# Optimization experiments

Hardware: AMD Instinct MI355X
Metric: run time of the kernel (lower is better)

Reference implementation:

```python
import math
import jax, jax.numpy as jnp
import numpy as np

B, H, S, D = 2, 16, 2048, 64


def setup_inputs() -> dict:
    key = jax.random.key(0)
    kq, kk, kv = jax.random.split(key, 3)
    Q = jax.random.normal(kq, (B, H, S, D), dtype=jnp.float32)
    K = jax.random.normal(kk, (B, H, S, D), dtype=jnp.float32)
    V = jax.random.normal(kv, (B, H, S, D), dtype=jnp.float32)
    # padding mask: (N, H, query_len), True = keep (module expands with [..., None])
    padding_mask = jnp.ones((B, H, S), dtype=bool)
    # boolean causal attention mask, broadcastable to (B, H, S, S)
    attention_mask = jnp.tril(jnp.ones((S, S), dtype=bool))[None, None]
    return {"Q": Q, "K": K, "V": V,
            "padding_mask": padding_mask, "attention_mask": attention_mask}


def reference(Q, K, V, padding_mask, attention_mask):
    # scores: (B, H, S_q, S_k)
    scale = 1.0 / math.sqrt(K.shape[-1])
    attn = jnp.einsum("bhqd,bhkd->bhqk", Q, K) * scale
    # query-side padding mask (is_query_mask=True): expand last axis
    attn = jnp.where(padding_mask[..., None], attn, -jnp.inf)
    # boolean attention mask
    attn = jnp.where(attention_mask, attn, -jnp.inf)
    attn = jax.nn.softmax(attn, axis=-1)
    # nan-clean: rows fully masked to -inf softmax to NaN -> 0
    attn = jnp.where(jnp.isnan(attn), 0.0, attn)
    return jnp.einsum("bhqk,bhkd->bhqd", attn, V)
```

## Files before the change

kernel.cpp:

```cpp
#include <hip/hip_runtime.h>


typedef __attribute__((ext_vector_type(8))) short bf16x8;
typedef __attribute__((ext_vector_type(4))) float f32x4;
typedef __attribute__((ext_vector_type(2))) unsigned uint2v;
typedef __attribute__((ext_vector_type(4))) unsigned uint4v;

#define MFMA16(a, b, c) __builtin_amdgcn_mfma_f32_16x16x32_bf16(a, b, c, 0, 0, 0)

#define S_LEN 2048
#define D_DIM 64
#define NBH 32

static __device__ __forceinline__ short f2bf(float f) {
  unsigned u = __builtin_bit_cast(unsigned, f);
  u += 0x7fffu + ((u >> 16) & 1u);
  return (short)(u >> 16);
}

static __device__ __forceinline__ unsigned pk2(float a, float b) {
#if __has_builtin(__builtin_amdgcn_cvt_pk_bf16_f32)
  auto r = __builtin_amdgcn_cvt_pk_bf16_f32(a, b);
  return __builtin_bit_cast(unsigned, r);
#else
  return (unsigned)(unsigned short)f2bf(a) |
         ((unsigned)(unsigned short)f2bf(b) << 16);
#endif
}

static __device__ __forceinline__ float fexp2(float x) {
#if __has_builtin(__builtin_amdgcn_exp2f)
  return __builtin_amdgcn_exp2f(x);
#else
  return exp2f(x);
#endif
}

static __device__ __forceinline__ bf16x8 cvt8(const float* p) {
  f32x4 a = *(const f32x4*)p;
  f32x4 b = *(const f32x4*)(p + 4);
  bf16x8 r;
#pragma unroll
  for (int j = 0; j < 4; ++j) { r[j] = f2bf(a[j]); r[j + 4] = f2bf(b[j]); }
  return r;
}

static __device__ __forceinline__ void load_lds16(const short* g, short* l) {
  __builtin_amdgcn_global_load_lds(
      (const __attribute__((address_space(1))) unsigned*)g,
      (__attribute__((address_space(3))) unsigned*)l, 16, 0, 0);
}

__global__ __launch_bounds__(256) void stage(const float* __restrict__ K,
                                             const float* __restrict__ V,
                                             short* __restrict__ Kb,
                                             short* __restrict__ Vt) {
  const int tid = threadIdx.x;
  if (blockIdx.x < 1024) {
    const size_t b0 = (size_t)blockIdx.x * 4096;
#pragma unroll
    for (int p = 0; p < 2; ++p) {
      const size_t i = b0 + p * 2048 + tid * 8;
      f32x4 a = *(const f32x4*)(K + i);
      f32x4 b = *(const f32x4*)(K + i + 4);
      bf16x8 r;
#pragma unroll
      for (int j = 0; j < 4; ++j) { r[j] = f2bf(a[j]); r[j + 4] = f2bf(b[j]); }
      *(bf16x8*)(Kb + i) = r;
    }
  } else {
    __shared__ unsigned t[64][18];
    const int bi = blockIdx.x - 1024;
    const int bh = bi >> 6, k32 = bi & 63;
    const float* src = V + ((size_t)bh * S_LEN + k32 * 32) * D_DIM;
    const int pr = tid & 15;
    const int dq = tid >> 4;
    f32x4 a = *(const f32x4*)(src + (2 * pr)     * D_DIM + dq * 4);
    f32x4 b = *(const f32x4*)(src + (2 * pr + 1) * D_DIM + dq * 4);
#pragma unroll
    for (int j = 0; j < 4; ++j) t[dq * 4 + j][pr] = pk2(a[j], b[j]);
    __syncthreads();
    const int d = tid >> 2, g = tid & 3;
    uint2v lo = *(const uint2v*)(&t[d][2 * g]);
    uint2v hi = *(const uint2v*)(&t[d][8 + 2 * g]);
    short* dst = Vt + (size_t)bh * D_DIM * S_LEN + (size_t)d * S_LEN +
                 k32 * 32 + g * 8;
    *(uint2v*)(dst)     = lo;
    *(uint2v*)(dst + 4) = hi;
  }
}

__global__ __launch_bounds__(512, 2) void attn_fwd(
    const float* __restrict__ Q, const short* __restrict__ Kb,
    const short* __restrict__ Vt, float* __restrict__ O) {
  __shared__ __align__(16) short kbuf[3][4096];
  __shared__ __align__(16) short vbuf[3][4096];

  const int tid  = threadIdx.x;
  const int wave = tid >> 6;
  const int cid  = wave >> 2;
  const int wq   = wave & 3;
  const int lane = tid & 63;
  const int quad = lane >> 4;
  const int col  = lane & 15;

  const int bh = blockIdx.x & 31;
  const int i2 = blockIdx.x >> 5;
  const int s = i2 & 7, g = i2 >> 3;
  const int p = g ? (15 - s) : s;
  const int qb   = 2 * p + cid;
  const int nblk = 2 * p + 2;
  const int q0 = qb * 64 + wq * 16;

  const float* Qh = Q  + (size_t)bh * S_LEN * D_DIM;
  const short* Kh = Kb + (size_t)bh * S_LEN * D_DIM;
  const short* Vh = Vt + (size_t)bh * D_DIM * S_LEN;

  const bf16x8 bq0 = cvt8(Qh + (size_t)(q0 + col) * D_DIM + quad * 8);
  const bf16x8 bq1 = cvt8(Qh + (size_t)(q0 + col) * D_DIM + quad * 8 + 32);

  const int r0s = tid >> 3, c0s = (tid & 7) ^ (r0s & 7);
  const int wb = wave * 512;

  f32x4 o[4];
#pragma unroll
  for (int i = 0; i < 4; ++i) o[i] = 0.f;
  float psum = 0.f;
  const float sc = 0.125f * 1.44269504088896340736f;

  const int rbase = col * 64;
  const int sw0 = ((quad       ^ (col & 7)) << 3);
  const int sw1 = (((4 + quad) ^ (col & 7)) << 3);

  auto prefetch = [&](int t, int buf) {
    const int k0n = t << 6;
    load_lds16(Kh + (size_t)(k0n + r0s) * 64 + c0s * 8, &kbuf[buf][wb]);
    load_lds16(Vh + (size_t)r0s * S_LEN + k0n + c0s * 8, &vbuf[buf][wb]);
  };

  auto body = [&](int t, bool masked, int buf) {
    const short* kb = kbuf[buf];
    const short* vb = vbuf[buf];

    bf16x8 ak0[4], ak1[4], av0[4], av1[4];
#pragma unroll
    for (int mt = 0; mt < 4; ++mt) {
      ak0[mt] = *(const bf16x8*)(kb + mt * 1024 + rbase + sw0);
      ak1[mt] = *(const bf16x8*)(kb + mt * 1024 + rbase + sw1);
    }
#pragma unroll
    for (int mt = 0; mt < 4; ++mt) {
      av0[mt] = *(const bf16x8*)(vb + mt * 1024 + rbase + sw0);
      av1[mt] = *(const bf16x8*)(vb + mt * 1024 + rbase + sw1);
    }

    f32x4 s4[4];
#pragma unroll
    for (int mt = 0; mt < 4; ++mt) {
      f32x4 c = 0.f;
      c = MFMA16(ak0[mt], bq0, c);
      c = MFMA16(ak1[mt], bq1, c);
      s4[mt] = c;
    }

    unsigned u[8];
    const int k0 = t << 6, qA = q0 + col;
#pragma unroll
    for (int mt = 0; mt < 4; ++mt) {
      float p0 = fexp2(fmaf(s4[mt][0], sc, -8.0f));
      float p1 = fexp2(fmaf(s4[mt][1], sc, -8.0f));
      float p2 = fexp2(fmaf(s4[mt][2], sc, -8.0f));
      float p3 = fexp2(fmaf(s4[mt][3], sc, -8.0f));
      if (masked) {
        const int kk = k0 + mt * 16 + quad * 4;
        if (kk     > qA) p0 = 0.f;
        if (kk + 1 > qA) p1 = 0.f;
        if (kk + 2 > qA) p2 = 0.f;
        if (kk + 3 > qA) p3 = 0.f;
      }
      psum += (p0 + p1) + (p2 + p3);
      u[2 * mt]     = pk2(p0, p1);
      u[2 * mt + 1] = pk2(p2, p3);
    }

    uint4v dv0, dv1;
    dv0[0] = u[0]; dv0[1] = u[1]; dv0[2] = u[2]; dv0[3] = u[3];
    dv1[0] = u[4]; dv1[1] = u[5]; dv1[2] = u[6]; dv1[3] = u[7];
    const bf16x8 bp0 = __builtin_bit_cast(bf16x8, dv0);
    const bf16x8 bp1 = __builtin_bit_cast(bf16x8, dv1);

#pragma unroll
    for (int mt = 0; mt < 4; ++mt) o[mt] = MFMA16(av0[mt], bp0, o[mt]);
#pragma unroll
    for (int mt = 0; mt < 4; ++mt) o[mt] = MFMA16(av1[mt], bp1, o[mt]);
  };

  prefetch(0, 0);
  prefetch(1, 1);
  int cur = 0;
  for (int t = 0; t < nblk; ++t) {
    if (t + 1 < nblk) {
      asm volatile("s_waitcnt vmcnt(2)" ::: "memory");
    } else {
      asm volatile("s_waitcnt vmcnt(0)" ::: "memory");
    }
    __builtin_amdgcn_s_barrier();
    if (t + 2 < nblk) {
      int nb = cur + 2; if (nb >= 3) nb -= 3;
      prefetch(t + 2, nb);
    }
    if (t <= qb) body(t, t == qb, cur);
    if (++cur == 3) cur = 0;
  }

  psum += __shfl_xor(psum, 16);
  psum += __shfl_xor(psum, 32);
  const float rl = 1.f / psum;
  float* op = O + (size_t)bh * S_LEN * D_DIM + (size_t)(q0 + col) * D_DIM;
#pragma unroll
  for (int mt = 0; mt < 4; ++mt) {
    f32x4 ov;
#pragma unroll
    for (int r = 0; r < 4; ++r) ov[r] = o[mt][r] * rl;
    *(f32x4*)(op + mt * 16 + quad * 4) = ov;
  }
}

extern "C" void kernel_launch(void* const* d_in, const int* in_sizes, int n_in,
                              void* d_out, int out_size, void* d_ws, size_t ws_size,
                              hipStream_t stream) {
  const float* Q = (const float*)d_in[0];
  const float* K = (const float*)d_in[1];
  const float* V = (const float*)d_in[2];
  short* Kb = (short*)d_ws;
  short* Vt = Kb + (size_t)NBH * S_LEN * D_DIM;
  stage   <<<dim3(3072), dim3(256), 0, stream>>>(K, V, Kb, Vt);
  attn_fwd<<<dim3(512),  dim3(512), 0, stream>>>(Q, Kb, Vt, (float*)d_out);
}
```

Before: 145.5 us.

## Software-pipeline QK^T one tile ahead with 4-deep LDS ring buffer

Splits the per-tile body into a QK^T stage and a softmax/PV stage, so the QK^T MFMAs for tile t+1 are issued before the exp and PV work of tile t, using ping-pong score registers. The LDS ring grows from 3 to 4 buffers and the prefetch distance from 2 to 3 tiles. The aim is to overlap MFMA work with the exp/convert work and to hide more global-to-LDS latency. In exchange it uses more LDS per block (64KB), which could limit the 2-blocks-per-CU occupancy, and it keeps more live registers.

Result: no change. 145.2 us (-0.2%).

```diff
diff --git a/kernel.cpp b/kernel.cpp
--- a/kernel.cpp
+++ b/kernel.cpp
@@ -93,8 +93,8 @@
 __global__ __launch_bounds__(512, 2) void attn_fwd(
     const float* __restrict__ Q, const short* __restrict__ Kb,
     const short* __restrict__ Vt, float* __restrict__ O) {
-  __shared__ __align__(16) short kbuf[3][4096];
-  __shared__ __align__(16) short vbuf[3][4096];
+  __shared__ __align__(16) short kbuf[4][4096];
+  __shared__ __align__(16) short vbuf[4][4096];
 
   const int tid  = threadIdx.x;
   const int wave = tid >> 6;
@@ -132,37 +132,35 @@
   const int sw0 = ((quad       ^ (col & 7)) << 3);
   const int sw1 = (((4 + quad) ^ (col & 7)) << 3);
 
-  auto prefetch = [&](int t, int buf) {
+  auto prefetch = [&](int t) {
     const int k0n = t << 6;
-    load_lds16(Kh + (size_t)(k0n + r0s) * 64 + c0s * 8, &kbuf[buf][wb]);
-    load_lds16(Vh + (size_t)r0s * S_LEN + k0n + c0s * 8, &vbuf[buf][wb]);
-  };
-
-  auto body = [&](int t, bool masked, int buf) {
-    const short* kb = kbuf[buf];
-    const short* vb = vbuf[buf];
-
-    bf16x8 ak0[4], ak1[4], av0[4], av1[4];
+    short* kd = &kbuf[t & 3][wb];
+    short* vd = &vbuf[t & 3][wb];
+    load_lds16(Kh + (size_t)(k0n + r0s) * 64 + c0s * 8, kd);
+    load_lds16(Vh + (size_t)r0s * S_LEN + k0n + c0s * 8, vd);
+  };
+
+  auto qk = [&](int t, f32x4 (&s4)[4]) {
+    const short* kb = kbuf[t & 3];
 #pragma unroll
     for (int mt = 0; mt < 4; ++mt) {
-      ak0[mt] = *(const bf16x8*)(kb + mt * 1024 + rbase + sw0);
-      ak1[mt] = *(const bf16x8*)(kb + mt * 1024 + rbase + sw1);
-    }
+      bf16x8 a0 = *(const bf16x8*)(kb + mt * 1024 + rbase + sw0);
+      bf16x8 a1 = *(const bf16x8*)(kb + mt * 1024 + rbase + sw1);
+      f32x4 c = 0.f;
+      c = MFMA16(a0, bq0, c);
+      c = MFMA16(a1, bq1, c);
+      s4[mt] = c;
+    }
+  };
+
+  auto fin = [&](int t, bool masked, const f32x4 (&s4)[4]) {
+    const short* vb = vbuf[t & 3];
+    bf16x8 av0[4], av1[4];
 #pragma unroll
     for (int mt = 0; mt < 4; ++mt) {
       av0[mt] = *(const bf16x8*)(vb + mt * 1024 + rbase + sw0);
       av1[mt] = *(const bf16x8*)(vb + mt * 1024 + rbase + sw1);
     }
-
-    f32x4 s4[4];
-#pragma unroll
-    for (int mt = 0; mt < 4; ++mt) {
-      f32x4 c = 0.f;
-      c = MFMA16(ak0[mt], bq0, c);
-      c = MFMA16(ak1[mt], bq1, c);
-      s4[mt] = c;
-    }
-
     unsigned u[8];
     const int k0 = t << 6, qA = q0 + col;
 #pragma unroll
@@ -182,35 +180,42 @@
       u[2 * mt]     = pk2(p0, p1);
       u[2 * mt + 1] = pk2(p2, p3);
     }
-
     uint4v dv0, dv1;
     dv0[0] = u[0]; dv0[1] = u[1]; dv0[2] = u[2]; dv0[3] = u[3];
     dv1[0] = u[4]; dv1[1] = u[5]; dv1[2] = u[6]; dv1[3] = u[7];
     const bf16x8 bp0 = __builtin_bit_cast(bf16x8, dv0);
     const bf16x8 bp1 = __builtin_bit_cast(bf16x8, dv1);
-
 #pragma unroll
     for (int mt = 0; mt < 4; ++mt) o[mt] = MFMA16(av0[mt], bp0, o[mt]);
 #pragma unroll
     for (int mt = 0; mt < 4; ++mt) o[mt] = MFMA16(av1[mt], bp1, o[mt]);
   };
 
-  prefetch(0, 0);
-  prefetch(1, 1);
-  int cur = 0;
-  for (int t = 0; t < nblk; ++t) {
-    if (t + 1 < nblk) {
+  auto step = [&](int t, const f32x4 (&scur)[4], f32x4 (&snext)[4]) {
+    if (t + 2 < nblk) {
       asm volatile("s_waitcnt vmcnt(2)" ::: "memory");
-    } else {
+    } else if (t + 1 < nblk) {
       asm volatile("s_waitcnt vmcnt(0)" ::: "memory");
     }
     __builtin_amdgcn_s_barrier();
-    if (t + 2 < nblk) {
-      int nb = cur + 2; if (nb >= 3) nb -= 3;
-      prefetch(t + 2, nb);
-    }
-    if (t <= qb) body(t, t == qb, cur);
-    if (++cur == 3) cur = 0;
+    if (t + 3 < nblk) prefetch(t + 3);
+    if (t + 1 <= qb) qk(t + 1, snext);
+    if (t <= qb) fin(t, t == qb, scur);
+  };
+
+  f32x4 sA[4], sB[4];
+  prefetch(0);
+  prefetch(1);
+  if (2 < nblk) prefetch(2);
+  if (2 < nblk) { asm volatile("s_waitcnt vmcnt(4)" ::: "memory"); }
+  else          { asm volatile("s_waitcnt vmcnt(2)" ::: "memory"); }
+  __builtin_amdgcn_s_barrier();
+  qk(0, sA);
+
+  int t = 0;
+  while (true) {
+    step(t, sA, sB); if (++t >= nblk) break;
+    step(t, sB, sA); if (++t >= nblk) break;
   }
 
   psum += __shfl_xor(psum, 16);
```
